# Performance work log

Measured on AMD Instinct MI355X. Metric: run time of the kernel, lower is better.

Reference implementation:

```python
import jax, jax.numpy as jnp
import numpy as np

R, N, B, S = 20, 4096, 16, 256          # relations, total nodes, graphs, nodes per graph
DIN, HID, H = 512, 128, 4               # in_dim, hidden_dim, num_heads
D = HID * H                              # flattened node-feature width (=512)
E = 16384                                # edges per relation
NEG_SLOPE = 0.2


def _gat(h, src, dst, W, al, ar, b):
    # DGL GATConv, eval mode (dropout off), identity residual (in == H*out), allow_zero_in_degree
    z = (h @ W).reshape(N, H, HID)                        # [N,H,Dh]
    el = (z * al).sum(-1)                                 # [N,H]
    er = (z * ar).sum(-1)                                 # [N,H]
    e = jax.nn.leaky_relu(el[src] + er[dst], NEG_SLOPE)   # [E,H]
    m = jax.ops.segment_max(e, dst, num_segments=N)       # per-dst max (edge softmax)
    ex = jnp.exp(e - m[dst])
    den = jax.ops.segment_sum(ex, dst, num_segments=N)
    alpha = ex / den[dst]                                 # [E,H]
    agg = jax.ops.segment_sum(alpha[..., None] * z[src], dst, num_segments=N)
    return agg + h.reshape(N, H, HID) + b, alpha


def _rgat_conv(h, src, dst, W, al, ar, b):
    # HeteroGraphConv with aggregate='mean' over R relations; scan keeps memory flat
    def body(acc, xs):
        s, d, Wr, alr, arr, br = xs
        out, alpha = _gat(h, s, d, Wr, alr, arr, br)
        return acc + out, alpha.mean(-1)                  # attention meaned over heads -> [E]
    acc, attn = jax.lax.scan(body, jnp.zeros((N, H, HID), h.dtype), (src, dst, W, al, ar, b))
    return acc / R, attn                                  # [N,H,Dh], [R,E]


def setup_inputs() -> dict:
    key = jax.random.key(0)
    ks = jax.random.split(key, 24)
    f32 = jnp.float32
    p = lambda k, shape: jax.random.normal(k, shape, f32) * 0.05
    z = lambda shape: jnp.zeros(shape, f32)
    return {
        'feat': jax.random.normal(ks[0], (N, DIN), f32),
        'hyp_emb': jax.random.normal(ks[1], (B, D), f32),
        'edge_src': jax.random.randint(ks[2], (R, E), 0, N),
        'edge_dst': jax.random.randint(ks[3], (R, E), 0, N),
        'W1': p(ks[4], (R, DIN, H * HID)), 'al1': p(ks[5], (R, H, HID)), 'ar1': p(ks[6], (R, H, HID)), 'b1': z((R, H, HID)),
        'W2': p(ks[7], (R, D, H * HID)), 'al2': p(ks[8], (R, H, HID)), 'ar2': p(ks[9], (R, H, HID)), 'b2': z((R, H, HID)),
        'Wq': p(ks[10], (D, D)), 'bq': z(D), 'Wk': p(ks[11], (D, D)), 'bk': z(D),
        'Wv': p(ks[12], (D, D)), 'bv': z(D), 'Wo': p(ks[13], (D, D)), 'bo': z(D),
        'Wn1': p(ks[14], (2 * D, HID)), 'bn1': z(HID), 'Wn2': p(ks[15], (HID, 2)), 'bn2': z(2),
    }


def reference(feat, hyp_emb, edge_src, edge_dst,
              W1, al1, ar1, b1, W2, al2, ar2, b2,
              Wq, bq, Wk, bk, Wv, bv, Wo, bo, Wn1, bn1, Wn2, bn2):
    # --- RGAT (rgat_generation) layer 1 + attention weights ---
    h1, attn = _rgat_conv(feat, edge_src, edge_dst, W1, al1, ar1, b1)
    h1 = jax.nn.elu(h1.reshape(N, D))
    # --- layer 2 ---
    h2, _ = _rgat_conv(h1, edge_src, edge_dst, W2, al2, ar2, b2)
    feats = h2.reshape(N, D)
    # --- node importance: scatter-add edge attention onto dst nodes, summed over etypes ---
    imp = jax.ops.segment_sum(attn.reshape(-1), edge_dst.reshape(-1), num_segments=N)
    feats_p = feats.reshape(B, S, D)                      # uniform graphs: split+pad == reshape
    weighted = feats_p * imp.reshape(B, S)[..., None]
    # --- MultiheadAttention(embed=D, heads=4): query = hyp_emb broadcast to all S positions ---
    Hm, Dm = 4, D // 4
    q = (hyp_emb @ Wq + bq).reshape(B, Hm, 1, Dm)         # identical query at every position
    k = (feats_p @ Wk + bk).reshape(B, S, Hm, Dm).transpose(0, 2, 1, 3)
    v = (feats_p @ Wv + bv).reshape(B, S, Hm, Dm).transpose(0, 2, 1, 3)
    scores = jnp.einsum('bhqd,bhkd->bhqk', q, k) / jnp.sqrt(jnp.float32(Dm))
    a = jax.nn.softmax(scores, axis=-1)                   # [B,Hm,1,S]
    ctx = jnp.einsum('bhqk,bhkd->bhqd', a, v).reshape(B, 1, D)
    attn_out = jnp.broadcast_to(ctx @ Wo + bo, (B, S, D))
    # --- node classifier on concat(weighted feats, attention output) ---
    combined = jnp.concatenate([weighted, attn_out], axis=-1).reshape(N, 2 * D)
    node_logits = jax.nn.relu(combined @ Wn1 + bn1) @ Wn2 + bn2
    return node_logits, attn
```

## Files before the change

kernel.cpp:

```cpp
#include <hip/hip_runtime.h>
#include <hip/hip_bf16.h>
#include <math.h>

#define NREL 20
#define NN   4096
#define NE   16384
#define DF   512
#define NHD  4
#define DHH  128
#define NB   16
#define NS   256

typedef __attribute__((ext_vector_type(8))) __bf16 bf16x8;
typedef __attribute__((ext_vector_type(4))) float f32x4;
typedef __attribute__((ext_vector_type(2))) float f32x2;

struct f8 { unsigned char b; };

__device__ inline float bf2f(unsigned short u) {
    union { float f; unsigned int i; } c; c.i = ((unsigned int)u) << 16; return c.f;
}
__device__ inline unsigned short f2bu(float f) {
    union { __hip_bfloat16 b; unsigned short u; } c; c.b = __float2bfloat16(f); return c.u;
}
__device__ inline void storeOut(float* p, float v) { *p = v; }
__device__ inline void storeOut(__hip_bfloat16* p, float v) { *p = __float2bfloat16(v); }

__device__ inline void load_lds16(const __hip_bfloat16* g, __hip_bfloat16* l) {
    __builtin_amdgcn_global_load_lds(
        (const __attribute__((address_space(1))) unsigned int*)(const void*)g,
        (__attribute__((address_space(3))) unsigned int*)(void*)l, 16, 0, 0);
}

__device__ inline int kswz(int f, int row) { return f ^ (((row) & 7) << 3); }

__global__ __launch_bounds__(256) void prep_kernel(
    const float* __restrict__ feat, unsigned short* __restrict__ featbf,
    const float* __restrict__ b1, const float* __restrict__ b2,
    const float* __restrict__ bk, const float* __restrict__ bv,
    float* __restrict__ bsum1, float* __restrict__ bsum2,
    float* __restrict__ bkv, int* __restrict__ cnt, float* __restrict__ imp)
{
    int blk = blockIdx.x, t = threadIdx.x;
    if (blk < 1024) {
        int idx = blk * 256 + t;
        int row = idx >> 6;
        int f = (idx & 63) * 8;
        int fs = kswz(f, row);
        const float4* ip = (const float4*)&feat[(size_t)row * DF + f];
        float4 v0 = ip[0], v1 = ip[1];
        union { unsigned short u[8]; uint4 q; } o;
        o.u[0] = f2bu(v0.x); o.u[1] = f2bu(v0.y); o.u[2] = f2bu(v0.z); o.u[3] = f2bu(v0.w);
        o.u[4] = f2bu(v1.x); o.u[5] = f2bu(v1.y); o.u[6] = f2bu(v1.z); o.u[7] = f2bu(v1.w);
        *(uint4*)(featbf + (size_t)row * DF + fs) = o.q;
    } else if (blk == 1024) {
        #pragma unroll
        for (int rep = 0; rep < 2; ++rep) {
            int f = t + rep * 256;
            float s1 = 0.f, s2 = 0.f;
            #pragma unroll
            for (int r = 0; r < NREL; ++r) { s1 += b1[r * DF + f]; s2 += b2[r * DF + f]; }
            bsum1[f] = s1; bsum2[f] = s2;
        }
        for (int i = t; i < NN; i += 256) imp[i] = 0.f;
    } else if (blk == 1025) {
        #pragma unroll
        for (int j = 0; j < 4; ++j) {
            int f = t + j * 256;
            bkv[f] = (f < DF) ? bk[f] : bv[f - DF];
        }
    } else {
        int idx = (blk - 1026) * 256 + t;
        cnt[idx] = 0;
    }
}

__global__ void count_kernel(const int* __restrict__ dst, int* __restrict__ cnt) {
    int idx = blockIdx.x * 256 + threadIdx.x;
    int r = idx / NE;
    atomicAdd(&cnt[r * NN + dst[idx]], 1);
}

__global__ void scan_kernel(const int* __restrict__ cnt, int* __restrict__ rowptr,
                            int* __restrict__ woff, int* __restrict__ rowptr2,
                            int* __restrict__ croff) {
    int r = blockIdx.x;
    int t = threadIdx.x;
    __shared__ int sums[1024];
    int v[4]; int local = 0;
    if (r < NREL) {
        #pragma unroll
        for (int j = 0; j < 4; ++j) { v[j] = cnt[r * NN + t * 4 + j]; local += v[j]; }
    } else {
        #pragma unroll
        for (int j = 0; j < 4; ++j) {
            int s = 0;
            for (int rel = 0; rel < NREL; ++rel) {
                croff[rel * NN + t * 4 + j] = s;
                s += cnt[rel * NN + t * 4 + j];
            }
            v[j] = s; local += s;
        }
    }
    sums[t] = local;
    __syncthreads();
    for (int off = 1; off < 1024; off <<= 1) {
        int x = (t >= off) ? sums[t - off] : 0;
        __syncthreads();
        sums[t] += x;
        __syncthreads();
    }
    int run = (t == 0) ? 0 : sums[t - 1];
    if (r < NREL) {
        #pragma unroll
        for (int j = 0; j < 4; ++j) {
            rowptr[r * (NN + 1) + t * 4 + j] = run;
            woff[r * NN + t * 4 + j] = run;
            run += v[j];
        }
        if (t == 1023) rowptr[r * (NN + 1) + NN] = run;
    } else {
        #pragma unroll
        for (int j = 0; j < 4; ++j) { rowptr2[t * 4 + j] = run; run += v[j]; }
        if (t == 1023) rowptr2[NN] = run;
    }
}

__global__ void fill_kernel(const int* __restrict__ dst, const int* __restrict__ src,
                            int* __restrict__ woff, int* __restrict__ srcCSR,
                            int* __restrict__ eidCSR) {
    int idx = blockIdx.x * 256 + threadIdx.x;
    int r = idx / NE; int e = idx % NE;
    int pos = atomicAdd(&woff[r * NN + dst[idx]], 1);
    srcCSR[r * NE + pos] = src[idx];
    eidCSR[r * NE + pos] = e;
}

__global__ __launch_bounds__(256) void transw_kernel(
    const float* __restrict__ W, __hip_bfloat16* __restrict__ Wt, int K, int N)
{
    int r = blockIdx.z;
    __shared__ float t[32][33];
    int k0 = blockIdx.x * 32, n0 = blockIdx.y * 32;
    int tx = threadIdx.x % 32, ty = threadIdx.x / 32;
    #pragma unroll
    for (int kk = ty; kk < 32; kk += 8)
        t[kk][tx] = W[((size_t)r * K + k0 + kk) * N + n0 + tx];
    __syncthreads();
    #pragma unroll
    for (int nn = ty; nn < 32; nn += 8) {
        int row = n0 + nn;
        Wt[((size_t)r * N + row) * K + kswz(k0 + tx, row)] = __float2bfloat16(t[tx][nn]);
    }
}

__global__ __launch_bounds__(256) void transw2_kernel(
    const float* __restrict__ W1, const float* __restrict__ W2,
    const float* __restrict__ Wk, const float* __restrict__ Wv,
    __hip_bfloat16* __restrict__ Wt1, __hip_bfloat16* __restrict__ Wt2,
    __hip_bfloat16* __restrict__ WtKV)
{
    int z = blockIdx.z;
    const float* Wsrc; __hip_bfloat16* Wdst;
    if (z < NREL)           { Wsrc = W1 + (size_t)z * DF * DF;          Wdst = Wt1 + (size_t)z * DF * DF; }
    else if (z < 2 * NREL)  { Wsrc = W2 + (size_t)(z - NREL) * DF * DF; Wdst = Wt2 + (size_t)(z - NREL) * DF * DF; }
    else if (z == 2 * NREL) { Wsrc = Wk;                                Wdst = WtKV; }
    else                    { Wsrc = Wv;                                Wdst = WtKV + (size_t)DF * DF; }
    __shared__ float t[32][33];
    int k0 = blockIdx.x * 32, n0 = blockIdx.y * 32;
    int tx = threadIdx.x % 32, ty = threadIdx.x / 32;
    #pragma unroll
    for (int kk = ty; kk < 32; kk += 8)
        t[kk][tx] = Wsrc[(size_t)(k0 + kk) * DF + n0 + tx];
    __syncthreads();
    #pragma unroll
    for (int nn = ty; nn < 32; nn += 8) {
        int row = n0 + nn;
        Wdst[(size_t)row * DF + kswz(k0 + tx, row)] = __float2bfloat16(t[tx][nn]);
    }
}

__global__ __launch_bounds__(1024) void zgemm16(
    const __hip_bfloat16* __restrict__ A,
    const __hip_bfloat16* __restrict__ BtAll,
    unsigned char* __restrict__ Zall,
    const float* __restrict__ al, const float* __restrict__ ar,
    float* __restrict__ el, float* __restrict__ er)
{
    const int r = blockIdx.z;
    const __hip_bfloat16* Bt = BtAll + (size_t)r * DF * DF;
    unsigned char* Z = Zall + (size_t)r * NN * DF;
    const int rowBase = blockIdx.y * 256;
    const int colBase = blockIdx.x * 256;
    __shared__ __hip_bfloat16 As[2][256][64];
    __shared__ __hip_bfloat16 Bs[2][256][64];
    const int tid = threadIdx.x;
    const int w = tid >> 6, l = tid & 63;
    const int wr = w >> 2, wc = w & 3;
    const int m15 = l & 15, q = l >> 4;
    const int swr = m15 & 7;

    const __hip_bfloat16* Ag = A + (size_t)(rowBase + (tid >> 3)) * DF + (tid & 7) * 8;
    const __hip_bfloat16* Bg = Bt + (size_t)(colBase + (tid >> 3)) * DF + (tid & 7) * 8;
    __hip_bfloat16* AsT = &As[0][0][0] + tid * 8;
    __hip_bfloat16* BsT = &Bs[0][0][0] + tid * 8;

#define STAGE_A(buf, kt) do { \
        const __hip_bfloat16* s_ = Ag + (kt) * 64; \
        __hip_bfloat16* d_ = AsT + (buf) * 16384; \
        load_lds16(s_, d_); \
        load_lds16(s_ + (size_t)128 * DF, d_ + 8192); } while (0)
#define STAGE_B(buf, kt) do { \
        const __hip_bfloat16* s_ = Bg + (kt) * 64; \
        __hip_bfloat16* d_ = BsT + (buf) * 16384; \
        load_lds16(s_, d_); \
        load_lds16(s_ + (size_t)128 * DF, d_ + 8192); } while (0)

    f32x4 acc[4][4];
    #pragma unroll
    for (int i = 0; i < 4; ++i)
        #pragma unroll
        for (int j = 0; j < 4; ++j) acc[i][j] = (f32x4){0.f, 0.f, 0.f, 0.f};

    const int NT = DF / 64;
    STAGE_A(0, 0); STAGE_B(0, 0);
    STAGE_A(1, 1); STAGE_B(1, 1);
    asm volatile("s_waitcnt vmcnt(4)" ::: "memory");
    __builtin_amdgcn_s_barrier();
    __builtin_amdgcn_sched_barrier(0);

    bf16x8 a[4], b[4];
    for (int kt = 0; kt < NT; ++kt) {
        const int buf = kt & 1;
        #pragma unroll
        for (int i = 0; i < 4; ++i)
            a[i] = *(const bf16x8*)&As[buf][wr * 64 + i * 16 + m15][(q ^ swr) * 8];
        #pragma unroll
        for (int j = 0; j < 4; ++j)
            b[j] = *(const bf16x8*)&Bs[buf][wc * 64 + j * 16 + m15][(q ^ swr) * 8];
        asm volatile("s_waitcnt lgkmcnt(0)" ::: "memory");
        __builtin_amdgcn_sched_barrier(0);
        __builtin_amdgcn_s_setprio(1);
        #pragma unroll
        for (int i = 0; i < 4; ++i)
            #pragma unroll
            for (int j = 0; j < 4; ++j)
                acc[i][j] = __builtin_amdgcn_mfma_f32_16x16x32_bf16(a[i], b[j], acc[i][j], 0, 0, 0);
        __builtin_amdgcn_s_setprio(0);
        #pragma unroll
        for (int i = 0; i < 4; ++i)
            a[i] = *(const bf16x8*)&As[buf][wr * 64 + i * 16 + m15][((4 + q) ^ swr) * 8];
        #pragma unroll
        for (int j = 0; j < 4; ++j)
            b[j] = *(const bf16x8*)&Bs[buf][wc * 64 + j * 16 + m15][((4 + q) ^ swr) * 8];
        asm volatile("s_waitcnt lgkmcnt(0)" ::: "memory");
        __builtin_amdgcn_sched_barrier(0);
        __builtin_amdgcn_s_barrier();
        __builtin_amdgcn_sched_barrier(0);
        if (kt + 2 < NT) { STAGE_A(buf, kt + 2); STAGE_B(buf, kt + 2); }
        __builtin_amdgcn_sched_barrier(0);
        __builtin_amdgcn_s_setprio(1);
        #pragma unroll
        for (int i = 0; i < 4; ++i)
            #pragma unroll
            for (int j = 0; j < 4; ++j)
                acc[i][j] = __builtin_amdgcn_mfma_f32_16x16x32_bf16(a[i], b[j], acc[i][j], 0, 0, 0);
        __builtin_amdgcn_s_setprio(0);
        if (kt + 2 < NT)      { asm volatile("s_waitcnt vmcnt(4)" ::: "memory"); }
        else if (kt + 1 < NT) { asm volatile("s_waitcnt vmcnt(0)" ::: "memory"); }
        __builtin_amdgcn_s_barrier();
        __builtin_amdgcn_sched_barrier(0);
    }
#undef STAGE_A
#undef STAGE_B

    unsigned char* cbuf = (unsigned char*)&As[0][0][0];
    #pragma unroll
    for (int i = 0; i < 4; ++i)
        #pragma unroll
        for (int j = 0; j < 4; ++j) {
            int colL = wc * 64 + j * 16 + m15;
            #pragma unroll
            for (int reg = 0; reg < 4; ++reg) {
                int rowL = wr * 64 + i * 16 + q * 4 + reg;
                unsigned int pk = __builtin_amdgcn_cvt_pk_fp8_f32(
                    acc[i][j][reg], acc[i][j][reg], 0, false);
                cbuf[rowL * 256 + colL] = (unsigned char)(pk & 0xFF);
            }
        }
    __syncthreads();
    {
        int rowL = tid >> 2, colL = (tid & 3) * 64;
        const uint4* src = (const uint4*)&cbuf[rowL * 256 + colL];
        uint4* dst = (uint4*)(Z + (size_t)(rowBase + rowL) * DF + colBase + colL);
        #pragma unroll
        for (int x = 0; x < 4; ++x) dst[x] = src[x];
    }

    float alv[4], arv[4];
    #pragma unroll
    for (int j = 0; j < 4; ++j) {
        int col = colBase + wc * 64 + j * 16 + m15;
        alv[j] = al[r * DF + col];
        arv[j] = ar[r * DF + col];
    }
    float pe[4][4], pr[4][4];
    #pragma unroll
    for (int i = 0; i < 4; ++i)
        #pragma unroll
        for (int reg = 0; reg < 4; ++reg) {
            float se = 0.f, sr = 0.f;
            #pragma unroll
            for (int j = 0; j < 4; ++j) {
                se += acc[i][j][reg] * alv[j];
                sr += acc[i][j][reg] * arv[j];
            }
            pe[i][reg] = se; pr[i][reg] = sr;
        }
    #pragma unroll
    for (int off = 1; off < 16; off <<= 1)
        #pragma unroll
        for (int i = 0; i < 4; ++i)
            #pragma unroll
            for (int reg = 0; reg < 4; ++reg) {
                pe[i][reg] += __shfl_xor(pe[i][reg], off);
                pr[i][reg] += __shfl_xor(pr[i][reg], off);
            }
    float* eP = (float*)&Bs[0][0][0];
    float* rP = eP + 1024;
    if (m15 == 0) {
        int hh = wc >> 1, strip = wc & 1;
        #pragma unroll
        for (int i = 0; i < 4; ++i)
            #pragma unroll
            for (int reg = 0; reg < 4; ++reg) {
                int rowL = wr * 64 + i * 16 + q * 4 + reg;
                eP[(hh * 256 + rowL) * 2 + strip] = pe[i][reg];
                rP[(hh * 256 + rowL) * 2 + strip] = pr[i][reg];
            }
    }
    __syncthreads();
    if (tid < 512) {
        int rowL = tid & 255, hh = tid >> 8;
        int head = (colBase >> 7) + hh;
        size_t idx = ((size_t)r * NN + rowBase + rowL) * NHD + head;
        el[idx] = eP[(hh * 256 + rowL) * 2] + eP[(hh * 256 + rowL) * 2 + 1];
        er[idx] = rP[(hh * 256 + rowL) * 2] + rP[(hh * 256 + rowL) * 2 + 1];
    }
}

template <typename OutT, bool RELU, bool FUSE, bool SPLITK = false>
__global__ __launch_bounds__(256) void mfma_gemm(
    const __hip_bfloat16* __restrict__ A,
    const __hip_bfloat16* __restrict__ BtAll,
    const float* __restrict__ bias, int biasStride,
    OutT* __restrict__ Call, int M, int N, int K, int lda,
    const float* __restrict__ al, const float* __restrict__ ar,
    float* __restrict__ el, float* __restrict__ er)
{
    int r = blockIdx.z;
    const __hip_bfloat16* Bt;
    int koff;
    if (SPLITK) { Bt = BtAll;                         koff = r * K; }
    else        { Bt = BtAll + (size_t)r * N * lda;   koff = 0; }
    OutT* C = Call + (size_t)r * M * N;
    const int rowBase = blockIdx.y * 128;
    const int colBase = blockIdx.x * 128;
    __shared__ __hip_bfloat16 As[128 * 64];
    __shared__ __hip_bfloat16 Bs[128 * 64];
    const int tid = threadIdx.x;
    const int w = tid >> 6, l = tid & 63;
    const int wr = w >> 1, wc = w & 1;
    const int m15 = l & 15, q = l >> 4;
    const int sRow = tid >> 3;
    const int sChk = tid & 7;
    const __hip_bfloat16* Ag = A + (size_t)(rowBase + sRow) * lda + koff + sChk * 8;
    const __hip_bfloat16* Bg = Bt + (size_t)(colBase + sRow) * lda + koff + sChk * 8;
    __hip_bfloat16* Asl = As + tid * 8;
    __hip_bfloat16* Bsl = Bs + tid * 8;
    const int swr = m15 & 7;

    f32x4 acc[4][4];
    #pragma unroll
    for (int i = 0; i < 4; ++i)
        #pragma unroll
        for (int j = 0; j < 4; ++j) acc[i][j] = (f32x4){0.f, 0.f, 0.f, 0.f};

    for (int k0 = 0; k0 < K; k0 += 64) {
        #pragma unroll
        for (int c = 0; c < 4; ++c) {
            load_lds16(Ag + (size_t)c * 32 * lda + k0, Asl + c * 2048);
            load_lds16(Bg + (size_t)c * 32 * lda + k0, Bsl + c * 2048);
        }
        __syncthreads();
        #pragma unroll
        for (int g = 0; g < 2; ++g) {
            bf16x8 a[4], b[4];
            #pragma unroll
            for (int i = 0; i < 4; ++i)
                a[i] = *(const bf16x8*)&As[(wr * 64 + i * 16 + m15) * 64 + ((g * 4 + q) ^ swr) * 8];
            #pragma unroll
            for (int j = 0; j < 4; ++j)
                b[j] = *(const bf16x8*)&Bs[(wc * 64 + j * 16 + m15) * 64 + ((g * 4 + q) ^ swr) * 8];
            #pragma unroll
            for (int i = 0; i < 4; ++i)
                #pragma unroll
                for (int j = 0; j < 4; ++j)
                    acc[i][j] = __builtin_amdgcn_mfma_f32_16x16x32_bf16(a[i], b[j], acc[i][j], 0, 0, 0);
        }
        __syncthreads();
    }

    if constexpr (sizeof(OutT) == 1) {
        unsigned char* cbuf = (unsigned char*)As;
        #pragma unroll
        for (int i = 0; i < 4; ++i)
            #pragma unroll
            for (int j = 0; j < 4; ++j) {
                int colL = wc * 64 + j * 16 + m15;
                #pragma unroll
                for (int reg = 0; reg < 4; ++reg) {
                    int rowL = wr * 64 + i * 16 + q * 4 + reg;
                    unsigned int pk = __builtin_amdgcn_cvt_pk_fp8_f32(
                        acc[i][j][reg], acc[i][j][reg], 0, false);
                    cbuf[rowL * 128 + colL] = (unsigned char)(pk & 0xFF);
                }
            }
        __syncthreads();
        int rowL = tid >> 1, colL = (tid & 1) * 64;
        const uint4* src = (const uint4*)&cbuf[rowL * 128 + colL];
        uint4* dst = (uint4*)((unsigned char*)C + (size_t)(rowBase + rowL) * N
                              + colBase + colL);
        #pragma unroll
        for (int x = 0; x < 4; ++x) dst[x] = src[x];
    } else {
        #pragma unroll
        for (int i = 0; i < 4; ++i) {
            #pragma unroll
            for (int j = 0; j < 4; ++j) {
                int col = colBase + wc * 64 + j * 16 + m15;
                float bv = bias ? bias[r * biasStride + col] : 0.f;
                #pragma unroll
                for (int reg = 0; reg < 4; ++reg) {
                    int row = rowBase + wr * 64 + i * 16 + q * 4 + reg;
                    float v = acc[i][j][reg] + bv;
                    if (RELU) v = fmaxf(v, 0.f);
                    storeOut(&C[(size_t)row * N + col], v);
                }
            }
        }
    }

    if (FUSE) {
        float alv[4], arv[4];
        #pragma unroll
        for (int j = 0; j < 4; ++j) {
            int col = colBase + wc * 64 + j * 16 + m15;
            alv[j] = al[r * DF + col];
            arv[j] = ar[r * DF + col];
        }
        float pe[4][4], pr[4][4];
        #pragma unroll
        for (int i = 0; i < 4; ++i)
            #pragma unroll
            for (int reg = 0; reg < 4; ++reg) {
                float se = 0.f, sr = 0.f;
                #pragma unroll
                for (int j = 0; j < 4; ++j) {
                    se += acc[i][j][reg] * alv[j];
                    sr += acc[i][j][reg] * arv[j];
                }
                pe[i][reg] = se; pr[i][reg] = sr;
            }
        #pragma unroll
        for (int off = 1; off < 16; off <<= 1)
            #pragma unroll
            for (int i = 0; i < 4; ++i)
                #pragma unroll
                for (int reg = 0; reg < 4; ++reg) {
                    pe[i][reg] += __shfl_xor(pe[i][reg], off);
                    pr[i][reg] += __shfl_xor(pr[i][reg], off);
                }
        float* eP = (float*)Bs;
        float* rP = eP + 256;
        if (m15 == 0) {
            #pragma unroll
            for (int i = 0; i < 4; ++i)
                #pragma unroll
                for (int reg = 0; reg < 4; ++reg) {
                    int rowL = wr * 64 + i * 16 + q * 4 + reg;
                    eP[rowL * 2 + wc] = pe[i][reg];
                    rP[rowL * 2 + wc] = pr[i][reg];
                }
        }
        __syncthreads();
        if (tid < 128) {
            int head = colBase >> 7;
            size_t idx = ((size_t)r * NN + rowBase + tid) * NHD + head;
            el[idx] = eP[tid * 2] + eP[tid * 2 + 1];
            er[idx] = rP[tid * 2] + rP[tid * 2 + 1];
        }
    }
}

template <typename OutT>
__global__ __launch_bounds__(256) void gemm_kernel(
    const float* __restrict__ A, const float* __restrict__ Bm,
    const float* __restrict__ bias, OutT* __restrict__ C,
    int M, int K, int Nn)
{
    int r = blockIdx.z;
    const float* B = Bm + (size_t)r * K * Nn;
    OutT* Cr = C + (size_t)r * M * Nn;
    int rowBase = blockIdx.y * 64;
    int colBase = blockIdx.x * 64;
    __shared__ float As[64][17];
    __shared__ float Bs[16][64];
    int tid = threadIdx.x;
    int tx = tid % 16, ty = tid / 16;
    float acc[4][4] = {};
    int aRow = tid / 4, aK4 = (tid % 4) * 4;
    int bK = tid / 16, bN4 = (tid % 16) * 4;
    for (int k0 = 0; k0 < K; k0 += 16) {
        int gRow = rowBase + aRow;
        float4 av = make_float4(0.f, 0.f, 0.f, 0.f);
        if (gRow < M) av = *(const float4*)(A + (size_t)gRow * K + k0 + aK4);
        As[aRow][aK4 + 0] = av.x; As[aRow][aK4 + 1] = av.y;
        As[aRow][aK4 + 2] = av.z; As[aRow][aK4 + 3] = av.w;
        float4 bv = *(const float4*)(B + (size_t)(k0 + bK) * Nn + colBase + bN4);
        *(float4*)&Bs[bK][bN4] = bv;
        __syncthreads();
        #pragma unroll
        for (int k = 0; k < 16; ++k) {
            float a[4], b[4];
            #pragma unroll
            for (int i = 0; i < 4; ++i) a[i] = As[ty * 4 + i][k];
            #pragma unroll
            for (int j = 0; j < 4; ++j) b[j] = Bs[k][tx * 4 + j];
            #pragma unroll
            for (int i = 0; i < 4; ++i)
                #pragma unroll
                for (int j = 0; j < 4; ++j) acc[i][j] += a[i] * b[j];
        }
        __syncthreads();
    }
    #pragma unroll
    for (int i = 0; i < 4; ++i) {
        int gRow = rowBase + ty * 4 + i;
        if (gRow >= M) continue;
        #pragma unroll
        for (int j = 0; j < 4; ++j) {
            int gCol = colBase + tx * 4 + j;
            float v = acc[i][j];
            if (bias) v += bias[gCol];
            storeOut(&Cr[(size_t)gRow * Nn + gCol], v);
        }
    }
}

__global__ __launch_bounds__(256) void alpha_kernel(
    const float* __restrict__ el, const float* __restrict__ er,
    const int* __restrict__ rowptr, const int* __restrict__ rowptr2,
    const int* __restrict__ croff, const int* __restrict__ srcCSR,
    const int* __restrict__ eidCSR,
    float* __restrict__ alphaPk, int* __restrict__ srcPk,
    float* __restrict__ attn, float* __restrict__ imp)
{
    int t = blockIdx.x * 256 + threadIdx.x;
    int r = t / NN, n = t % NN;
    int start = rowptr[r * (NN + 1) + n];
    int d = rowptr[r * (NN + 1) + n + 1] - start;
    if (d == 0) return;
    int pbase = rowptr2[n] + croff[r * NN + n];
    float4 er4 = *(const float4*)&er[((size_t)r * NN + n) * NHD];
    float4 den = make_float4(0.f, 0.f, 0.f, 0.f);
    for (int j = 0; j < d; ++j) {
        int s = srcCSR[r * NE + start + j];
        float4 el4 = *(const float4*)&el[((size_t)r * NN + s) * NHD];
        float v0 = el4.x + er4.x; v0 = v0 > 0.f ? v0 : 0.2f * v0;
        float v1 = el4.y + er4.y; v1 = v1 > 0.f ? v1 : 0.2f * v1;
        float v2 = el4.z + er4.z; v2 = v2 > 0.f ? v2 : 0.2f * v2;
        float v3 = el4.w + er4.w; v3 = v3 > 0.f ? v3 : 0.2f * v3;
        float4 e4 = make_float4(__expf(v0), __expf(v1), __expf(v2), __expf(v3));
        den.x += e4.x; den.y += e4.y; den.z += e4.z; den.w += e4.w;
        *(float4*)&alphaPk[(size_t)(pbase + j) * 4] = e4;
        srcPk[pbase + j] = r * NN + s;
    }
    float4 inv = make_float4(1.f / den.x, 1.f / den.y, 1.f / den.z, 1.f / den.w);
    float impLoc = 0.f;
    for (int j = 0; j < d; ++j) {
        float4 a4 = *(const float4*)&alphaPk[(size_t)(pbase + j) * 4];
        a4.x *= inv.x; a4.y *= inv.y; a4.z *= inv.z; a4.w *= inv.w;
        *(float4*)&alphaPk[(size_t)(pbase + j) * 4] = a4;
        if (attn) {
            float a = 0.25f * (a4.x + a4.y + a4.z + a4.w);
            attn[r * NE + eidCSR[r * NE + start + j]] = a;
            impLoc += a;
        }
    }
    if (attn) atomicAdd(&imp[n], impLoc);
}

__global__ __launch_bounds__(256) void aggc_kernel(
    const unsigned char* __restrict__ Z,
    const int* __restrict__ rowptr2, const int* __restrict__ srcPk,
    const float* __restrict__ alphaPk, const float* __restrict__ bsum,
    const float* __restrict__ hin, float* __restrict__ hout,
    __hip_bfloat16* __restrict__ hout_bf, int applyElu)
{
    int n = blockIdx.x;
    int w = threadIdx.x >> 6, lane = threadIdx.x & 63;
    int h = lane >> 4;
    int base = rowptr2[n];
    int deg = rowptr2[n + 1] - base;
    float acc[8] = {};
    if (deg > 0) {
        int i = w * 4;
        int zz[4]; float aa[4];
        #pragma unroll
        for (int j = 0; j < 4; ++j) {
            int idx = i + j; int cidx = idx < deg ? idx : deg - 1;
            zz[j] = srcPk[base + cidx];
            aa[j] = (idx < deg) ? alphaPk[(size_t)(base + cidx) * 4 + h] : 0.f;
        }
        while (i < deg) {
            int cz[4]; float ca[4];
            #pragma unroll
            for (int j = 0; j < 4; ++j) { cz[j] = zz[j]; ca[j] = aa[j]; }
            int ni = i + 16;
            #pragma unroll
            for (int j = 0; j < 4; ++j) {
                int idx = ni + j; int cidx = idx < deg ? idx : deg - 1;
                zz[j] = srcPk[base + cidx];
                aa[j] = (idx < deg) ? alphaPk[(size_t)(base + cidx) * 4 + h] : 0.f;
            }
            uint2 raw[4];
            #pragma unroll
            for (int j = 0; j < 4; ++j)
                raw[j] = *(const uint2*)&Z[(size_t)cz[j] * DF + lane * 8];
            #pragma unroll
            for (int j = 0; j < 4; ++j) {
                f32x2 f01 = __builtin_amdgcn_cvt_pk_f32_fp8((int)raw[j].x, false);
                f32x2 f23 = __builtin_amdgcn_cvt_pk_f32_fp8((int)raw[j].x, true);
                f32x2 f45 = __builtin_amdgcn_cvt_pk_f32_fp8((int)raw[j].y, false);
                f32x2 f67 = __builtin_amdgcn_cvt_pk_f32_fp8((int)raw[j].y, true);
                acc[0] += ca[j] * f01.x; acc[1] += ca[j] * f01.y;
                acc[2] += ca[j] * f23.x; acc[3] += ca[j] * f23.y;
                acc[4] += ca[j] * f45.x; acc[5] += ca[j] * f45.y;
                acc[6] += ca[j] * f67.x; acc[7] += ca[j] * f67.y;
            }
            i = ni;
        }
    }
    __shared__ float red[4][DF];
    #pragma unroll
    for (int j = 0; j < 8; ++j) red[w][lane * 8 + j] = acc[j];
    __syncthreads();
    const float invR = 1.0f / NREL;
    const int sw = (n & 7) << 3;
    int f = threadIdx.x;
    #pragma unroll
    for (int rep = 0; rep < 2; ++rep, f += 256) {
        float v = red[0][f] + red[1][f] + red[2][f] + red[3][f];
        v = (v + bsum[f]) * invR + hin[(size_t)n * DF + f];
        if (applyElu) v = v > 0.f ? v : expm1f(v);
        hout[(size_t)n * DF + f] = v;
        hout_bf[(size_t)n * DF + (f ^ sw)] = __float2bfloat16(v);
    }
}

__global__ __launch_bounds__(256) void mha_scores(
    const float* __restrict__ q, const float* __restrict__ k,
    float* __restrict__ scores)
{
    int b = blockIdx.x;
    int w = threadIdx.x >> 6, lane = threadIdx.x & 63;
    int s = blockIdx.y * 4 + w;
    const float4* qp = (const float4*)&q[(size_t)b * DF + lane * 8];
    const float4* kp = (const float4*)&k[((size_t)(b * NS + s)) * DF + lane * 8];
    float4 q0 = qp[0], q1 = qp[1];
    float4 k0 = kp[0], k1 = kp[1];
    float p = q0.x * k0.x + q0.y * k0.y + q0.z * k0.z + q0.w * k0.w
            + q1.x * k1.x + q1.y * k1.y + q1.z * k1.z + q1.w * k1.w;
    #pragma unroll
    for (int off = 1; off < 16; off <<= 1) p += __shfl_xor(p, off);
    if ((lane & 15) == 0) {
        int h = lane >> 4;
        scores[((size_t)(b * NHD + h)) * NS + s] = p * 0.08838834764831845f;
    }
}

__global__ __launch_bounds__(256) void mha_ctx(
    const float* __restrict__ scores, const float* __restrict__ v,
    float* __restrict__ ctx)
{
    int b = blockIdx.x, h = blockIdx.y;
    int t = threadIdx.x;
    int lane = t & 63, w = t >> 6;
    __shared__ float a_s[NS];
    __shared__ float wred[8];
    float sv = scores[((size_t)(b * NHD + h)) * NS + t];
    float mx = sv;
    #pragma unroll
    for (int off = 1; off < 64; off <<= 1) mx = fmaxf(mx, __shfl_xor(mx, off));
    if (lane == 0) wred[w] = mx;
    __syncthreads();
    mx = fmaxf(fmaxf(wred[0], wred[1]), fmaxf(wred[2], wred[3]));
    float e = __expf(sv - mx);
    float sum = e;
    #pragma unroll
    for (int off = 1; off < 64; off <<= 1) sum += __shfl_xor(sum, off);
    if (lane == 0) wred[4 + w] = sum;
    __syncthreads();
    sum = wred[4] + wred[5] + wred[6] + wred[7];
    a_s[t] = e * (1.0f / sum);
    __syncthreads();
    int d = t & 127, half = t >> 7;
    float acc = 0.f;
    const float* vp = &v[((size_t)(b * NS + half * 128)) * DF + h * DHH + d];
    #pragma unroll 4
    for (int i = 0; i < 128; ++i)
        acc += a_s[half * 128 + i] * vp[(size_t)i * DF];
    __shared__ float red[256];
    red[t] = acc;
    __syncthreads();
    if (t < 128) ctx[(size_t)b * DF + h * DHH + t] = red[t] + red[t + 128];
}

__global__ __launch_bounds__(256) void combined_kernel(
    const float* __restrict__ feats, const float* __restrict__ imp,
    const float* __restrict__ abuf, __hip_bfloat16* __restrict__ comb)
{
    int n = blockIdx.x;
    int t = threadIdx.x;
    int b = n >> 8;
    float im = imp[n];
    const int sw = (n & 7) << 3;
    #pragma unroll
    for (int rep = 0; rep < 4; ++rep) {
        int f = t + rep * 256;
        float v = (f < DF) ? feats[(size_t)n * DF + f] * im
                           : abuf[(size_t)b * DF + (f - DF)];
        comb[(size_t)n * (2 * DF) + (f ^ sw)] = __float2bfloat16(v);
    }
}

__global__ __launch_bounds__(256) void cls2_kernel(
    const float* __restrict__ hidden4, const float* __restrict__ bn1,
    const float* __restrict__ Wn2, const float* __restrict__ bn2,
    float* __restrict__ out)
{
    __shared__ float w2[256];
    __shared__ float b1s[128];
    int t = threadIdx.x;
    w2[t] = Wn2[t];
    if (t < 128) b1s[t] = bn1[t];
    __syncthreads();
    int n = blockIdx.x * 256 + t;
    const float* hp = &hidden4[(size_t)n * 128];
    const size_t ps = (size_t)NN * 128;
    float p0 = bn2[0], p1 = bn2[1];
    #pragma unroll 4
    for (int kk = 0; kk < 128; ++kk) {
        float hv = hp[kk] + hp[ps + kk] + hp[2 * ps + kk] + hp[3 * ps + kk] + b1s[kk];
        hv = fmaxf(hv, 0.f);
        p0 += hv * w2[kk * 2 + 0];
        p1 += hv * w2[kk * 2 + 1];
    }
    out[n * 2 + 0] = p0;
    out[n * 2 + 1] = p1;
}

extern "C" void kernel_launch(void* const* d_in, const int* in_sizes, int n_in,
                              void* d_out, int out_size, void* d_ws, size_t ws_size,
                              hipStream_t stream) {
    const float* feat = (const float*)d_in[0];
    const float* hyp  = (const float*)d_in[1];
    const int*   esrc = (const int*)d_in[2];
    const int*   edst = (const int*)d_in[3];
    const float* W1   = (const float*)d_in[4];
    const float* al1  = (const float*)d_in[5];
    const float* ar1  = (const float*)d_in[6];
    const float* b1   = (const float*)d_in[7];
    const float* W2   = (const float*)d_in[8];
    const float* al2  = (const float*)d_in[9];
    const float* ar2  = (const float*)d_in[10];
    const float* b2   = (const float*)d_in[11];
    const float* Wq = (const float*)d_in[12]; const float* bq = (const float*)d_in[13];
    const float* Wk = (const float*)d_in[14]; const float* bk = (const float*)d_in[15];
    const float* Wv = (const float*)d_in[16]; const float* bv = (const float*)d_in[17];
    const float* Wo = (const float*)d_in[18]; const float* bo = (const float*)d_in[19];
    const float* Wn1 = (const float*)d_in[20]; const float* bn1 = (const float*)d_in[21];
    const float* Wn2 = (const float*)d_in[22]; const float* bn2 = (const float*)d_in[23];

    char* ws = (char*)d_ws;
    size_t off = 0;
    auto alloc = [&](size_t bytes) -> void* {
        void* p = ws + off;
        off += (bytes + 255) & ~(size_t)255;
        return p;
    };
    unsigned char* Z = (unsigned char*)alloc((size_t)NREL * NN * DF);
    float* el     = (float*)alloc((size_t)NREL * NN * NHD * 4);
    float* er     = (float*)alloc((size_t)NREL * NN * NHD * 4);
    int* rowptr   = (int*)alloc((size_t)NREL * (NN + 1) * 4);
    int* rowptr2  = (int*)alloc((size_t)(NN + 1) * 4);
    int* woff     = (int*)alloc((size_t)NREL * NN * 4);
    int* srcCSR   = (int*)alloc((size_t)NREL * NE * 4);
    int* eidCSR   = (int*)alloc((size_t)NREL * NE * 4);
    int* cnt      = (int*)alloc((size_t)NREL * NN * 4);
    int* croff    = (int*)alloc((size_t)NREL * NN * 4);
    int* srcPk    = (int*)alloc((size_t)NREL * NE * 4);
    float* alphaPk= (float*)alloc((size_t)NREL * NE * NHD * 4);
    float* bsum1  = (float*)alloc((size_t)DF * 4);
    float* bsum2  = (float*)alloc((size_t)DF * 4);
    float* bkv    = (float*)alloc((size_t)2 * DF * 4);
    float* h1     = (float*)alloc((size_t)NN * DF * 4);
    float* feats  = (float*)alloc((size_t)NN * DF * 4);
    float* imp    = (float*)alloc((size_t)NN * 4);
    float* kvbuf  = (float*)alloc((size_t)2 * NN * DF * 4);
    float* qbuf   = (float*)alloc((size_t)NB * DF * 4);
    float* ctxb   = (float*)alloc((size_t)NB * DF * 4);
    float* abuf   = (float*)alloc((size_t)NB * DF * 4);
    float* scoresb= (float*)alloc((size_t)NB * NHD * NS * 4);
    float* hidden4= (float*)alloc((size_t)4 * NN * 128 * 4);
    __hip_bfloat16* featbf  = (__hip_bfloat16*)alloc((size_t)NN * DF * 2);
    __hip_bfloat16* h1bf    = (__hip_bfloat16*)alloc((size_t)NN * DF * 2);
    __hip_bfloat16* featsbf = (__hip_bfloat16*)alloc((size_t)NN * DF * 2);
    __hip_bfloat16* combbf  = (__hip_bfloat16*)alloc((size_t)NN * 2 * DF * 2);
    __hip_bfloat16* Wt1 = (__hip_bfloat16*)alloc((size_t)NREL * DF * DF * 2);
    __hip_bfloat16* Wt2 = (__hip_bfloat16*)alloc((size_t)NREL * DF * DF * 2);
    __hip_bfloat16* WtKV = (__hip_bfloat16*)alloc((size_t)2 * DF * DF * 2);
    __hip_bfloat16* Wn1t = (__hip_bfloat16*)alloc((size_t)(2 * DF) * 128 * 2);
    if (off > ws_size) return;

    float* logits = (float*)d_out;
    float* attn   = (float*)d_out + (size_t)NN * 2;
    float* kbuf = kvbuf;
    float* vbuf = kvbuf + (size_t)NN * DF;

    prep_kernel<<<1026 + NREL * NN / 256, 256, 0, stream>>>(
        feat, (unsigned short*)featbf, b1, b2, bk, bv, bsum1, bsum2, bkv, cnt, imp);

    count_kernel<<<NREL * NE / 256, 256, 0, stream>>>(edst, cnt);
    scan_kernel<<<NREL + 1, 1024, 0, stream>>>(cnt, rowptr, woff, rowptr2, croff);
    fill_kernel<<<NREL * NE / 256, 256, 0, stream>>>(edst, esrc, woff, srcCSR, eidCSR);

    transw2_kernel<<<dim3(DF / 32, DF / 32, 2 * NREL + 2), 256, 0, stream>>>(
        W1, W2, Wk, Wv, Wt1, Wt2, WtKV);
    transw_kernel<<<dim3(2 * DF / 32, 128 / 32, 1), 256, 0, stream>>>(Wn1, Wn1t, 2 * DF, 128);

    zgemm16<<<dim3(DF / 256, NN / 256, NREL), 1024, 0, stream>>>(
        featbf, Wt1, Z, al1, ar1, el, er);
    alpha_kernel<<<NREL * NN / 256, 256, 0, stream>>>(
        el, er, rowptr, rowptr2, croff, srcCSR, eidCSR, alphaPk, srcPk, attn, imp);
    aggc_kernel<<<NN, 256, 0, stream>>>(Z, rowptr2, srcPk, alphaPk, bsum1,
                                        feat, h1, h1bf, 1);

    zgemm16<<<dim3(DF / 256, NN / 256, NREL), 1024, 0, stream>>>(
        h1bf, Wt2, Z, al2, ar2, el, er);
    alpha_kernel<<<NREL * NN / 256, 256, 0, stream>>>(
        el, er, rowptr, rowptr2, croff, srcCSR, eidCSR, alphaPk, srcPk, nullptr, nullptr);
    aggc_kernel<<<NN, 256, 0, stream>>>(Z, rowptr2, srcPk, alphaPk, bsum2,
                                        h1, feats, featsbf, 0);

    mfma_gemm<float, false, false><<<dim3(DF / 128, NN / 128, 2), 256, 0, stream>>>(
        featsbf, WtKV, bkv, DF, kvbuf, NN, DF, DF, DF, nullptr, nullptr, nullptr, nullptr);
    gemm_kernel<float><<<dim3(DF / 64, 1, 1), 256, 0, stream>>>(
        hyp, Wq, bq, qbuf, NB, DF, DF);
    mha_scores<<<dim3(NB, NS / 4), 256, 0, stream>>>(qbuf, kbuf, scoresb);
    mha_ctx<<<dim3(NB, NHD), 256, 0, stream>>>(scoresb, vbuf, ctxb);
    gemm_kernel<float><<<dim3(DF / 64, 1, 1), 256, 0, stream>>>(
        ctxb, Wo, bo, abuf, NB, DF, DF);

    combined_kernel<<<NN, 256, 0, stream>>>(feats, imp, abuf, combbf);
    mfma_gemm<float, false, false, true><<<dim3(1, NN / 128, 4), 256, 0, stream>>>(
        combbf, Wn1t, nullptr, 0, hidden4, NN, 128, 256, 2 * DF,
        nullptr, nullptr, nullptr, nullptr);
    cls2_kernel<<<NN / 256, 256, 0, stream>>>(hidden4, bn1, Wn2, bn2, logits);
}
```

Before: 563.8 us.

## Narrow Z-GEMM tile to 256x128 with triple-buffered LDS, split classifier reduction

```diff
diff --git a/kernel.cpp b/kernel.cpp
--- a/kernel.cpp
+++ b/kernel.cpp
@@ -180,7 +180,7 @@
     }
 }
 
-__global__ __launch_bounds__(1024) void zgemm16(
+__global__ __launch_bounds__(1024) void zgemm3(
     const __hip_bfloat16* __restrict__ A,
     const __hip_bfloat16* __restrict__ BtAll,
     unsigned char* __restrict__ Zall,
@@ -191,9 +191,9 @@
     const __hip_bfloat16* Bt = BtAll + (size_t)r * DF * DF;
     unsigned char* Z = Zall + (size_t)r * NN * DF;
     const int rowBase = blockIdx.y * 256;
-    const int colBase = blockIdx.x * 256;
-    __shared__ __hip_bfloat16 As[2][256][64];
-    __shared__ __hip_bfloat16 Bs[2][256][64];
+    const int colBase = blockIdx.x * 128;
+    __shared__ __hip_bfloat16 As[3][256][64];
+    __shared__ __hip_bfloat16 Bs[3][128][64];
     const int tid = threadIdx.x;
     const int w = tid >> 6, l = tid & 63;
     const int wr = w >> 2, wc = w & 3;
@@ -211,62 +211,61 @@
         load_lds16(s_, d_); \
         load_lds16(s_ + (size_t)128 * DF, d_ + 8192); } while (0)
 #define STAGE_B(buf, kt) do { \
-        const __hip_bfloat16* s_ = Bg + (kt) * 64; \
-        __hip_bfloat16* d_ = BsT + (buf) * 16384; \
-        load_lds16(s_, d_); \
-        load_lds16(s_ + (size_t)128 * DF, d_ + 8192); } while (0)
-
-    f32x4 acc[4][4];
+        load_lds16(Bg + (kt) * 64, BsT + (buf) * 8192); } while (0)
+
+    f32x4 acc[4][2];
     #pragma unroll
     for (int i = 0; i < 4; ++i)
         #pragma unroll
-        for (int j = 0; j < 4; ++j) acc[i][j] = (f32x4){0.f, 0.f, 0.f, 0.f};
+        for (int j = 0; j < 2; ++j) acc[i][j] = (f32x4){0.f, 0.f, 0.f, 0.f};
 
     const int NT = DF / 64;
     STAGE_A(0, 0); STAGE_B(0, 0);
     STAGE_A(1, 1); STAGE_B(1, 1);
-    asm volatile("s_waitcnt vmcnt(4)" ::: "memory");
+    asm volatile("s_waitcnt vmcnt(3)" ::: "memory");
     __builtin_amdgcn_s_barrier();
     __builtin_amdgcn_sched_barrier(0);
 
-    bf16x8 a[4], b[4];
+    bf16x8 a[4], b[2];
+    #pragma unroll
     for (int kt = 0; kt < NT; ++kt) {
-        const int buf = kt & 1;
+        const int buf = kt % 3;
+        if (kt + 2 < NT) {
+            const int sb = (kt + 2) % 3;
+            STAGE_A(sb, kt + 2); STAGE_B(sb, kt + 2);
+        }
+        __builtin_amdgcn_sched_barrier(0);
         #pragma unroll
         for (int i = 0; i < 4; ++i)
             a[i] = *(const bf16x8*)&As[buf][wr * 64 + i * 16 + m15][(q ^ swr) * 8];
         #pragma unroll
-        for (int j = 0; j < 4; ++j)
-            b[j] = *(const bf16x8*)&Bs[buf][wc * 64 + j * 16 + m15][(q ^ swr) * 8];
+        for (int j = 0; j < 2; ++j)
+            b[j] = *(const bf16x8*)&Bs[buf][wc * 32 + j * 16 + m15][(q ^ swr) * 8];
         asm volatile("s_waitcnt lgkmcnt(0)" ::: "memory");
         __builtin_amdgcn_sched_barrier(0);
         __builtin_amdgcn_s_setprio(1);
         #pragma unroll
         for (int i = 0; i < 4; ++i)
             #pragma unroll
-            for (int j = 0; j < 4; ++j)
+            for (int j = 0; j < 2; ++j)
                 acc[i][j] = __builtin_amdgcn_mfma_f32_16x16x32_bf16(a[i], b[j], acc[i][j], 0, 0, 0);
         __builtin_amdgcn_s_setprio(0);
         #pragma unroll
         for (int i = 0; i < 4; ++i)
             a[i] = *(const bf16x8*)&As[buf][wr * 64 + i * 16 + m15][((4 + q) ^ swr) * 8];
         #pragma unroll
-        for (int j = 0; j < 4; ++j)
-            b[j] = *(const bf16x8*)&Bs[buf][wc * 64 + j * 16 + m15][((4 + q) ^ swr) * 8];
+        for (int j = 0; j < 2; ++j)
+            b[j] = *(const bf16x8*)&Bs[buf][wc * 32 + j * 16 + m15][((4 + q) ^ swr) * 8];
         asm volatile("s_waitcnt lgkmcnt(0)" ::: "memory");
         __builtin_amdgcn_sched_barrier(0);
-        __builtin_amdgcn_s_barrier();
-        __builtin_amdgcn_sched_barrier(0);
-        if (kt + 2 < NT) { STAGE_A(buf, kt + 2); STAGE_B(buf, kt + 2); }
-        __builtin_amdgcn_sched_barrier(0);
         __builtin_amdgcn_s_setprio(1);
         #pragma unroll
         for (int i = 0; i < 4; ++i)
             #pragma unroll
-            for (int j = 0; j < 4; ++j)
+            for (int j = 0; j < 2; ++j)
                 acc[i][j] = __builtin_amdgcn_mfma_f32_16x16x32_bf16(a[i], b[j], acc[i][j], 0, 0, 0);
         __builtin_amdgcn_s_setprio(0);
-        if (kt + 2 < NT)      { asm volatile("s_waitcnt vmcnt(4)" ::: "memory"); }
+        if (kt + 2 < NT)      { asm volatile("s_waitcnt vmcnt(3)" ::: "memory"); }
         else if (kt + 1 < NT) { asm volatile("s_waitcnt vmcnt(0)" ::: "memory"); }
         __builtin_amdgcn_s_barrier();
         __builtin_amdgcn_sched_barrier(0);
@@ -278,29 +277,28 @@
     #pragma unroll
     for (int i = 0; i < 4; ++i)
         #pragma unroll
-        for (int j = 0; j < 4; ++j) {
-            int colL = wc * 64 + j * 16 + m15;
+        for (int j = 0; j < 2; ++j) {
+            int colL = wc * 32 + j * 16 + m15;
             #pragma unroll
             for (int reg = 0; reg < 4; ++reg) {
                 int rowL = wr * 64 + i * 16 + q * 4 + reg;
                 unsigned int pk = __builtin_amdgcn_cvt_pk_fp8_f32(
                     acc[i][j][reg], acc[i][j][reg], 0, false);
-                cbuf[rowL * 256 + colL] = (unsigned char)(pk & 0xFF);
+                cbuf[rowL * 128 + colL] = (unsigned char)(pk & 0xFF);
             }
         }
     __syncthreads();
     {
-        int rowL = tid >> 2, colL = (tid & 3) * 64;
-        const uint4* src = (const uint4*)&cbuf[rowL * 256 + colL];
+        int rowL = tid >> 2, colL = (tid & 3) * 32;
+        const uint4* src = (const uint4*)&cbuf[rowL * 128 + colL];
         uint4* dst = (uint4*)(Z + (size_t)(rowBase + rowL) * DF + colBase + colL);
-        #pragma unroll
-        for (int x = 0; x < 4; ++x) dst[x] = src[x];
-    }
-
-    float alv[4], arv[4];
-    #pragma unroll
-    for (int j = 0; j < 4; ++j) {
-        int col = colBase + wc * 64 + j * 16 + m15;
+        dst[0] = src[0]; dst[1] = src[1];
+    }
+
+    float alv[2], arv[2];
+    #pragma unroll
+    for (int j = 0; j < 2; ++j) {
+        int col = colBase + wc * 32 + j * 16 + m15;
         alv[j] = al[r * DF + col];
         arv[j] = ar[r * DF + col];
     }
@@ -311,7 +309,7 @@
         for (int reg = 0; reg < 4; ++reg) {
             float se = 0.f, sr = 0.f;
             #pragma unroll
-            for (int j = 0; j < 4; ++j) {
+            for (int j = 0; j < 2; ++j) {
                 se += acc[i][j][reg] * alv[j];
                 sr += acc[i][j][reg] * arv[j];
             }
@@ -329,23 +327,21 @@
     float* eP = (float*)&Bs[0][0][0];
     float* rP = eP + 1024;
     if (m15 == 0) {
-        int hh = wc >> 1, strip = wc & 1;
         #pragma unroll
         for (int i = 0; i < 4; ++i)
             #pragma unroll
             for (int reg = 0; reg < 4; ++reg) {
                 int rowL = wr * 64 + i * 16 + q * 4 + reg;
-                eP[(hh * 256 + rowL) * 2 + strip] = pe[i][reg];
-                rP[(hh * 256 + rowL) * 2 + strip] = pr[i][reg];
-            }
-    }
-    __syncthreads();
-    if (tid < 512) {
-        int rowL = tid & 255, hh = tid >> 8;
-        int head = (colBase >> 7) + hh;
-        size_t idx = ((size_t)r * NN + rowBase + rowL) * NHD + head;
-        el[idx] = eP[(hh * 256 + rowL) * 2] + eP[(hh * 256 + rowL) * 2 + 1];
-        er[idx] = rP[(hh * 256 + rowL) * 2] + rP[(hh * 256 + rowL) * 2 + 1];
+                eP[rowL * 4 + wc] = pe[i][reg];
+                rP[rowL * 4 + wc] = pr[i][reg];
+            }
+    }
+    __syncthreads();
+    if (tid < 256) {
+        int head = colBase >> 7;
+        size_t idx = ((size_t)r * NN + rowBase + tid) * NHD + head;
+        el[idx] = (eP[tid * 4] + eP[tid * 4 + 1]) + (eP[tid * 4 + 2] + eP[tid * 4 + 3]);
+        er[idx] = (rP[tid * 4] + rP[tid * 4 + 1]) + (rP[tid * 4 + 2] + rP[tid * 4 + 3]);
     }
 }
 
@@ -756,19 +752,25 @@
     w2[t] = Wn2[t];
     if (t < 128) b1s[t] = bn1[t];
     __syncthreads();
-    int n = blockIdx.x * 256 + t;
+    int n = blockIdx.x * 64 + (t >> 2);
+    int tq = t & 3;
     const float* hp = &hidden4[(size_t)n * 128];
     const size_t ps = (size_t)NN * 128;
-    float p0 = bn2[0], p1 = bn2[1];
+    float p0 = 0.f, p1 = 0.f;
+    int k0 = tq * 32;
     #pragma unroll 4
-    for (int kk = 0; kk < 128; ++kk) {
+    for (int kk = k0; kk < k0 + 32; ++kk) {
         float hv = hp[kk] + hp[ps + kk] + hp[2 * ps + kk] + hp[3 * ps + kk] + b1s[kk];
         hv = fmaxf(hv, 0.f);
         p0 += hv * w2[kk * 2 + 0];
         p1 += hv * w2[kk * 2 + 1];
     }
-    out[n * 2 + 0] = p0;
-    out[n * 2 + 1] = p1;
+    p0 += __shfl_xor(p0, 1); p0 += __shfl_xor(p0, 2);
+    p1 += __shfl_xor(p1, 1); p1 += __shfl_xor(p1, 2);
+    if (tq == 0) {
+        out[n * 2 + 0] = p0 + bn2[0];
+        out[n * 2 + 1] = p1 + bn2[1];
+    }
 }
 
 extern "C" void kernel_launch(void* const* d_in, const int* in_sizes, int n_in,
@@ -850,14 +852,14 @@
         W1, W2, Wk, Wv, Wt1, Wt2, WtKV);
     transw_kernel<<<dim3(2 * DF / 32, 128 / 32, 1), 256, 0, stream>>>(Wn1, Wn1t, 2 * DF, 128);
 
-    zgemm16<<<dim3(DF / 256, NN / 256, NREL), 1024, 0, stream>>>(
+    zgemm3<<<dim3(DF / 128, NN / 256, NREL), 1024, 0, stream>>>(
         featbf, Wt1, Z, al1, ar1, el, er);
     alpha_kernel<<<NREL * NN / 256, 256, 0, stream>>>(
         el, er, rowptr, rowptr2, croff, srcCSR, eidCSR, alphaPk, srcPk, attn, imp);
     aggc_kernel<<<NN, 256, 0, stream>>>(Z, rowptr2, srcPk, alphaPk, bsum1,
                                         feat, h1, h1bf, 1);
 
-    zgemm16<<<dim3(DF / 256, NN / 256, NREL), 1024, 0, stream>>>(
+    zgemm3<<<dim3(DF / 128, NN / 256, NREL), 1024, 0, stream>>>(
         h1bf, Wt2, Z, al2, ar2, el, er);
     alpha_kernel<<<NREL * NN / 256, 256, 0, stream>>>(
         el, er, rowptr, rowptr2, croff, srcCSR, eidCSR, alphaPk, srcPk, nullptr, nullptr);
@@ -877,5 +879,5 @@
     mfma_gemm<float, false, false, true><<<dim3(1, NN / 128, 4), 256, 0, stream>>>(
         combbf, Wn1t, nullptr, 0, hidden4, NN, 128, 256, 2 * DF,
         nullptr, nullptr, nullptr, nullptr);
-    cls2_kernel<<<NN / 256, 256, 0, stream>>>(hidden4, bn1, Wn2, bn2, logits);
-}
+    cls2_kernel<<<NN / 64, 256, 0, stream>>>(hidden4, bn1, Wn2, bn2, logits);
+}
```

Result: slower. 590.4 us (+4.7%).

## Halve zgemm K-tile to 32, shrink LDS footprint, and split cls2 reduction across lanes

Applied to the files above, without the earlier changes.

```diff
diff --git a/kernel.cpp b/kernel.cpp
--- a/kernel.cpp
+++ b/kernel.cpp
@@ -32,7 +32,7 @@
         (__attribute__((address_space(3))) unsigned int*)(void*)l, 16, 0, 0);
 }
 
-__device__ inline int kswz(int f, int row) { return f ^ (((row) & 7) << 3); }
+__device__ inline int kswz(int f, int row) { return f ^ ((((row) >> 1) & 3) << 3); }
 
 __global__ __launch_bounds__(256) void prep_kernel(
     const float* __restrict__ feat, unsigned short* __restrict__ featbf,
@@ -180,7 +180,7 @@
     }
 }
 
-__global__ __launch_bounds__(1024) void zgemm16(
+__global__ __launch_bounds__(1024) void zgemmd(
     const __hip_bfloat16* __restrict__ A,
     const __hip_bfloat16* __restrict__ BtAll,
     unsigned char* __restrict__ Zall,
@@ -192,29 +192,22 @@
     unsigned char* Z = Zall + (size_t)r * NN * DF;
     const int rowBase = blockIdx.y * 256;
     const int colBase = blockIdx.x * 256;
-    __shared__ __hip_bfloat16 As[2][256][64];
-    __shared__ __hip_bfloat16 Bs[2][256][64];
+    __shared__ __hip_bfloat16 lds[32768];
     const int tid = threadIdx.x;
     const int w = tid >> 6, l = tid & 63;
     const int wr = w >> 2, wc = w & 3;
     const int m15 = l & 15, q = l >> 4;
-    const int swr = m15 & 7;
-
-    const __hip_bfloat16* Ag = A + (size_t)(rowBase + (tid >> 3)) * DF + (tid & 7) * 8;
-    const __hip_bfloat16* Bg = Bt + (size_t)(colBase + (tid >> 3)) * DF + (tid & 7) * 8;
-    __hip_bfloat16* AsT = &As[0][0][0] + tid * 8;
-    __hip_bfloat16* BsT = &Bs[0][0][0] + tid * 8;
-
-#define STAGE_A(buf, kt) do { \
-        const __hip_bfloat16* s_ = Ag + (kt) * 64; \
-        __hip_bfloat16* d_ = AsT + (buf) * 16384; \
-        load_lds16(s_, d_); \
-        load_lds16(s_ + (size_t)128 * DF, d_ + 8192); } while (0)
-#define STAGE_B(buf, kt) do { \
-        const __hip_bfloat16* s_ = Bg + (kt) * 64; \
-        __hip_bfloat16* d_ = BsT + (buf) * 16384; \
-        load_lds16(s_, d_); \
-        load_lds16(s_ + (size_t)128 * DF, d_ + 8192); } while (0)
+    const int swr = (m15 >> 1) & 3;
+
+    const int sRow = tid >> 2;
+    const __hip_bfloat16* Ag = A + (size_t)(rowBase + sRow) * DF + (tid & 3) * 8;
+    const __hip_bfloat16* Bg = Bt + (size_t)(colBase + sRow) * DF + (tid & 3) * 8;
+    __hip_bfloat16* AsT = lds + tid * 8;
+    __hip_bfloat16* BsT = lds + 16384 + tid * 8;
+
+#define STAGE(buf, kt) do { \
+        load_lds16(Ag + (kt) * 32, AsT + (buf) * 8192); \
+        load_lds16(Bg + (kt) * 32, BsT + (buf) * 8192); } while (0)
 
     f32x4 acc[4][4];
     #pragma unroll
@@ -222,42 +215,28 @@
         #pragma unroll
         for (int j = 0; j < 4; ++j) acc[i][j] = (f32x4){0.f, 0.f, 0.f, 0.f};
 
-    const int NT = DF / 64;
-    STAGE_A(0, 0); STAGE_B(0, 0);
-    STAGE_A(1, 1); STAGE_B(1, 1);
-    asm volatile("s_waitcnt vmcnt(4)" ::: "memory");
+    const int NT = DF / 32;
+    STAGE(0, 0); STAGE(1, 1);
+    asm volatile("s_waitcnt vmcnt(2)" ::: "memory");
     __builtin_amdgcn_s_barrier();
     __builtin_amdgcn_sched_barrier(0);
 
     bf16x8 a[4], b[4];
     for (int kt = 0; kt < NT; ++kt) {
         const int buf = kt & 1;
+        const int aOff = buf * 8192;
+        const int bOff = 16384 + buf * 8192;
         #pragma unroll
         for (int i = 0; i < 4; ++i)
-            a[i] = *(const bf16x8*)&As[buf][wr * 64 + i * 16 + m15][(q ^ swr) * 8];
+            a[i] = *(const bf16x8*)&lds[aOff + (wr * 64 + i * 16 + m15) * 32 + (q ^ swr) * 8];
         #pragma unroll
         for (int j = 0; j < 4; ++j)
-            b[j] = *(const bf16x8*)&Bs[buf][wc * 64 + j * 16 + m15][(q ^ swr) * 8];
-        asm volatile("s_waitcnt lgkmcnt(0)" ::: "memory");
-        __builtin_amdgcn_sched_barrier(0);
-        __builtin_amdgcn_s_setprio(1);
-        #pragma unroll
-        for (int i = 0; i < 4; ++i)
-            #pragma unroll
-            for (int j = 0; j < 4; ++j)
-                acc[i][j] = __builtin_amdgcn_mfma_f32_16x16x32_bf16(a[i], b[j], acc[i][j], 0, 0, 0);
-        __builtin_amdgcn_s_setprio(0);
-        #pragma unroll
-        for (int i = 0; i < 4; ++i)
-            a[i] = *(const bf16x8*)&As[buf][wr * 64 + i * 16 + m15][((4 + q) ^ swr) * 8];
-        #pragma unroll
-        for (int j = 0; j < 4; ++j)
-            b[j] = *(const bf16x8*)&Bs[buf][wc * 64 + j * 16 + m15][((4 + q) ^ swr) * 8];
+            b[j] = *(const bf16x8*)&lds[bOff + (wc * 64 + j * 16 + m15) * 32 + (q ^ swr) * 8];
         asm volatile("s_waitcnt lgkmcnt(0)" ::: "memory");
         __builtin_amdgcn_sched_barrier(0);
         __builtin_amdgcn_s_barrier();
         __builtin_amdgcn_sched_barrier(0);
-        if (kt + 2 < NT) { STAGE_A(buf, kt + 2); STAGE_B(buf, kt + 2); }
+        if (kt + 2 < NT) STAGE(buf, kt + 2);
         __builtin_amdgcn_sched_barrier(0);
         __builtin_amdgcn_s_setprio(1);
         #pragma unroll
@@ -266,15 +245,14 @@
             for (int j = 0; j < 4; ++j)
                 acc[i][j] = __builtin_amdgcn_mfma_f32_16x16x32_bf16(a[i], b[j], acc[i][j], 0, 0, 0);
         __builtin_amdgcn_s_setprio(0);
-        if (kt + 2 < NT)      { asm volatile("s_waitcnt vmcnt(4)" ::: "memory"); }
+        if (kt + 2 < NT)      { asm volatile("s_waitcnt vmcnt(2)" ::: "memory"); }
         else if (kt + 1 < NT) { asm volatile("s_waitcnt vmcnt(0)" ::: "memory"); }
         __builtin_amdgcn_s_barrier();
         __builtin_amdgcn_sched_barrier(0);
     }
-#undef STAGE_A
-#undef STAGE_B
-
-    unsigned char* cbuf = (unsigned char*)&As[0][0][0];
+#undef STAGE
+
+    unsigned char* cbuf = (unsigned char*)lds;
     #pragma unroll
     for (int i = 0; i < 4; ++i)
         #pragma unroll
@@ -296,6 +274,7 @@
         #pragma unroll
         for (int x = 0; x < 4; ++x) dst[x] = src[x];
     }
+    __syncthreads();
 
     float alv[4], arv[4];
     #pragma unroll
@@ -326,7 +305,7 @@
                 pe[i][reg] += __shfl_xor(pe[i][reg], off);
                 pr[i][reg] += __shfl_xor(pr[i][reg], off);
             }
-    float* eP = (float*)&Bs[0][0][0];
+    float* eP = (float*)lds;
     float* rP = eP + 1024;
     if (m15 == 0) {
         int hh = wc >> 1, strip = wc & 1;
@@ -378,7 +357,7 @@
     const __hip_bfloat16* Bg = Bt + (size_t)(colBase + sRow) * lda + koff + sChk * 8;
     __hip_bfloat16* Asl = As + tid * 8;
     __hip_bfloat16* Bsl = Bs + tid * 8;
-    const int swr = m15 & 7;
+    const int swr = (m15 >> 1) & 3;
 
     f32x4 acc[4][4];
     #pragma unroll
@@ -657,7 +636,7 @@
     for (int j = 0; j < 8; ++j) red[w][lane * 8 + j] = acc[j];
     __syncthreads();
     const float invR = 1.0f / NREL;
-    const int sw = (n & 7) << 3;
+    const int sw = ((n >> 1) & 3) << 3;
     int f = threadIdx.x;
     #pragma unroll
     for (int rep = 0; rep < 2; ++rep, f += 256) {
@@ -735,7 +714,7 @@
     int t = threadIdx.x;
     int b = n >> 8;
     float im = imp[n];
-    const int sw = (n & 7) << 3;
+    const int sw = ((n >> 1) & 3) << 3;
     #pragma unroll
     for (int rep = 0; rep < 4; ++rep) {
         int f = t + rep * 256;
@@ -756,19 +735,25 @@
     w2[t] = Wn2[t];
     if (t < 128) b1s[t] = bn1[t];
     __syncthreads();
-    int n = blockIdx.x * 256 + t;
+    int n = blockIdx.x * 64 + (t >> 2);
+    int tq = t & 3;
     const float* hp = &hidden4[(size_t)n * 128];
     const size_t ps = (size_t)NN * 128;
-    float p0 = bn2[0], p1 = bn2[1];
+    float p0 = 0.f, p1 = 0.f;
+    int k0 = tq * 32;
     #pragma unroll 4
-    for (int kk = 0; kk < 128; ++kk) {
+    for (int kk = k0; kk < k0 + 32; ++kk) {
         float hv = hp[kk] + hp[ps + kk] + hp[2 * ps + kk] + hp[3 * ps + kk] + b1s[kk];
         hv = fmaxf(hv, 0.f);
         p0 += hv * w2[kk * 2 + 0];
         p1 += hv * w2[kk * 2 + 1];
     }
-    out[n * 2 + 0] = p0;
-    out[n * 2 + 1] = p1;
+    p0 += __shfl_xor(p0, 1); p0 += __shfl_xor(p0, 2);
+    p1 += __shfl_xor(p1, 1); p1 += __shfl_xor(p1, 2);
+    if (tq == 0) {
+        out[n * 2 + 0] = p0 + bn2[0];
+        out[n * 2 + 1] = p1 + bn2[1];
+    }
 }
 
 extern "C" void kernel_launch(void* const* d_in, const int* in_sizes, int n_in,
@@ -850,14 +835,14 @@
         W1, W2, Wk, Wv, Wt1, Wt2, WtKV);
     transw_kernel<<<dim3(2 * DF / 32, 128 / 32, 1), 256, 0, stream>>>(Wn1, Wn1t, 2 * DF, 128);
 
-    zgemm16<<<dim3(DF / 256, NN / 256, NREL), 1024, 0, stream>>>(
+    zgemmd<<<dim3(DF / 256, NN / 256, NREL), 1024, 0, stream>>>(
         featbf, Wt1, Z, al1, ar1, el, er);
     alpha_kernel<<<NREL * NN / 256, 256, 0, stream>>>(
         el, er, rowptr, rowptr2, croff, srcCSR, eidCSR, alphaPk, srcPk, attn, imp);
     aggc_kernel<<<NN, 256, 0, stream>>>(Z, rowptr2, srcPk, alphaPk, bsum1,
                                         feat, h1, h1bf, 1);
 
-    zgemm16<<<dim3(DF / 256, NN / 256, NREL), 1024, 0, stream>>>(
+    zgemmd<<<dim3(DF / 256, NN / 256, NREL), 1024, 0, stream>>>(
         h1bf, Wt2, Z, al2, ar2, el, er);
     alpha_kernel<<<NREL * NN / 256, 256, 0, stream>>>(
         el, er, rowptr, rowptr2, croff, srcCSR, eidCSR, alphaPk, srcPk, nullptr, nullptr);
@@ -877,5 +862,5 @@
     mfma_gemm<float, false, false, true><<<dim3(1, NN / 128, 4), 256, 0, stream>>>(
         combbf, Wn1t, nullptr, 0, hidden4, NN, 128, 256, 2 * DF,
         nullptr, nullptr, nullptr, nullptr);
-    cls2_kernel<<<NN / 256, 256, 0, stream>>>(hidden4, bn1, Wn2, bn2, logits);
-}
+    cls2_kernel<<<NN / 64, 256, 0, stream>>>(hidden4, bn1, Wn2, bn2, logits);
+}
```

Result: slower. 579.9 us (+2.9%).
